# Optimization experiments

Measured on AMD Instinct MI355X. Metric: run time of the kernel, lower is better.

The kernel has to match this reference:

```python
import jax, jax.numpy as jnp
from jax import lax
import numpy as np

DIM = 96
D_STATE = 16
D_CONV = 4
EXPAND = 2
D_INNER = EXPAND * DIM


def _layernorm(x, g, b, eps=1e-5):
    mu = jnp.mean(x, axis=-1, keepdims=True)
    var = jnp.var(x, axis=-1, keepdims=True)
    return (x - mu) * lax.rsqrt(var + eps) * g + b


def _pssm(x, Wp, cw, cb, A, Dp, Wo):
    # x: (B, L, C)
    Bn, L, _ = x.shape
    xp = x @ Wp                                  # (B, L, 3*d_inner)
    x_conv, delta, BC = jnp.split(xp, 3, axis=-1)
    # causal depthwise conv1d (torch pads d_conv-1 both sides then slices [:L] == left pad)
    xc = lax.conv_general_dilated(
        jnp.transpose(x_conv, (0, 2, 1)), cw, (1,), [(D_CONV - 1, 0)],
        dimension_numbers=('NCH', 'OIH', 'NCH'), feature_group_count=D_INNER)
    xc = jnp.transpose(xc, (0, 2, 1)) + cb       # (B, L, d_inner)
    delta = jax.nn.sigmoid(delta)                # (B, L, d_inner)
    Bm = BC[..., :D_STATE]                       # (B, L, N) input gate
    Cm = BC[..., D_STATE:2 * D_STATE]            # (B, L, N) output gate
    # literal einsum 'bnl,ij->bnil' sums A over j -> row-sums vector
    Asum = jnp.sum(A, axis=1)                    # (N,)
    a = jnp.exp(delta[:, :, None, :] * Asum[None, None, :, None])   # (B,L,N,d)
    bu = (delta * xc)[:, :, None, :] * Bm[..., None]                 # (B,L,N,d)

    def scan_dir(a_, b_):
        def step(h, ab):
            at, bt = ab
            h = at * h + bt
            return h, h
        _, hs = lax.scan(step, jnp.zeros_like(a_[:, 0]),
                         (jnp.moveaxis(a_, 1, 0), jnp.moveaxis(b_, 1, 0)))
        return jnp.moveaxis(hs, 0, 1)            # (B, L, N, d)

    h = scan_dir(a, bu) + scan_dir(a[:, ::-1], bu[:, ::-1])[:, ::-1]
    y = jnp.einsum('blnd,bln->bld', h, Cm) + Dp * xc
    return y @ Wo                                # (B, L, C)


def _forward(x, norm_g, norm_b,
             Wp1, cw1, cb1, A1, Dp1, Wo1, lng1, lnb1,
             Wp2, cw2, cb2, A2, Dp2, Wo2, lng2, lnb2,
             Wf, bf, W1, b1, W2, b2):
    Bn, H, W_, C = x.shape
    res = x
    xn = _layernorm(x, norm_g, norm_b)
    xs = xn.reshape(Bn, H * W_, C)
    f1 = _layernorm(_pssm(xs, Wp1, cw1, cb1, A1, Dp1, Wo1), lng1, lnb1).reshape(Bn, H, W_, C)
    f2 = _layernorm(_pssm(xs, Wp2, cw2, cb2, A2, Dp2, Wo2), lng2, lnb2).reshape(Bn, H, W_, C)
    EPS = 1e-12
    n1 = f1 / jnp.maximum(jnp.linalg.norm(f1, axis=-1, keepdims=True), EPS)
    n2 = f2 / jnp.maximum(jnp.linalg.norm(f2, axis=-1, keepdims=True), EPS)
    sim = jnp.sum(n1 * n2, axis=-1, keepdims=True)          # (B,H,W,1)
    fused = sim * f1 + (1.0 - sim) * f2
    cat = jnp.concatenate([f1, fused], axis=-1)             # (B,H,W,2C)
    fc = lax.conv_general_dilated(cat, Wf, (1, 1), 'SAME',
                                  dimension_numbers=('NHWC', 'HWIO', 'NHWC')) + bf
    fc = jax.nn.gelu(fc, approximate=False)
    y = jax.nn.gelu(fc @ W1 + b1, approximate=False) @ W2 + b2
    return y + res


def setup_inputs() -> dict:
    key = jax.random.key(0)
    ks = jax.random.split(key, 32)
    B, H, W, C = 2, 64, 64, DIM

    def n(k, shape, s=1.0):
        return jax.random.normal(k, shape, dtype=jnp.float32) * s

    inp = {}
    inp['x'] = n(ks[0], (B, H, W, C))
    inp['norm_g'] = jnp.ones((C,), jnp.float32)
    inp['norm_b'] = jnp.zeros((C,), jnp.float32)
    for i, off in enumerate([1, 10]):
        p = str(i + 1)
        inp['Wp' + p] = n(ks[off], (C, 3 * D_INNER), 0.02)
        inp['cw' + p] = n(ks[off + 1], (D_INNER, 1, D_CONV), 0.1)
        inp['cb' + p] = jnp.zeros((D_INNER,), jnp.float32)
        # negative A row-sums keep exp(delta*Asum) < 1 -> stable scan over L=4096
        inp['A' + p] = -jnp.abs(n(ks[off + 2], (D_STATE, D_STATE))) * 0.1
        inp['Dp' + p] = n(ks[off + 3], (D_INNER,), 0.1)
        inp['Wo' + p] = n(ks[off + 4], (D_INNER, C), 0.02)
        inp['lng' + p] = jnp.ones((C,), jnp.float32)
        inp['lnb' + p] = jnp.zeros((C,), jnp.float32)
    inp['Wf'] = n(ks[20], (3, 3, 2 * C, C), 0.02)
    inp['bf'] = jnp.zeros((C,), jnp.float32)
    inp['W1'] = n(ks[21], (C, 4 * C), 0.02)
    inp['b1'] = jnp.zeros((4 * C,), jnp.float32)
    inp['W2'] = n(ks[22], (4 * C, C), 0.02)
    inp['b2'] = jnp.zeros((C,), jnp.float32)
    return inp


def reference(x, norm_g, norm_b,
              Wp1, cw1, cb1, A1, Dp1, Wo1, lng1, lnb1,
              Wp2, cw2, cb2, A2, Dp2, Wo2, lng2, lnb2,
              Wf, bf, W1, b1, W2, b2):
    return _forward(x, norm_g, norm_b,
                    Wp1, cw1, cb1, A1, Dp1, Wo1, lng1, lnb1,
                    Wp2, cw2, cb2, A2, Dp2, Wo2, lng2, lnb2,
                    Wf, bf, W1, b1, W2, b2)
```

## Files before the change

kernel.cpp:

```cpp
#include <hip/hip_runtime.h>
#include <hip/hip_bf16.h>
#include <math.h>

#define L_SEQ 4096
#define CDIM 96
#define DIN 192
#define NST 16
#define NCHUNK 64
#define CHLEN 64
#define MROWS 8192
#define XPW2 960
#define SCAN_GRID 3072

typedef __attribute__((ext_vector_type(8))) short bf16x8;
typedef __attribute__((ext_vector_type(4))) float f32x4;
typedef __attribute__((ext_vector_type(4))) short s16x4;
typedef __attribute__((ext_vector_type(4))) unsigned short u16x4;

__device__ __forceinline__ float gelu_exact(float x) {
    return 0.5f * x * (1.0f + erff(x * 0.70710678118654752f));
}

__device__ __forceinline__ float fast_exp2(float x) {
#if __has_builtin(__builtin_amdgcn_exp2f)
    return __builtin_amdgcn_exp2f(x);
#else
    return exp2f(x);
#endif
}

__device__ __forceinline__ float b2f(unsigned short u) {
    return __uint_as_float((unsigned int)u << 16);
}

__device__ __forceinline__ float rowsum16(float s) {
    asm("v_add_f32_dpp %0, %0, %0 row_ror:8 row_mask:0xf bank_mask:0xf" : "+v"(s));
    asm("v_add_f32_dpp %0, %0, %0 row_ror:4 row_mask:0xf bank_mask:0xf" : "+v"(s));
    asm("v_add_f32_dpp %0, %0, %0 row_ror:2 row_mask:0xf bank_mask:0xf" : "+v"(s));
    asm("v_add_f32_dpp %0, %0, %0 row_ror:1 row_mask:0xf bank_mask:0xf" : "+v"(s));
    return s;
}

__device__ __forceinline__ unsigned short f2bf_bits(float f) {
    __hip_bfloat16 h = __float2bfloat16(f);
    return *reinterpret_cast<unsigned short*>(&h);
}

#define CVT_BLOCKS 1440
__global__ __launch_bounds__(256) void prep_kernel(
    const float* __restrict__ Wp0, const float* __restrict__ Wp1,
    const float* __restrict__ Wo0, const float* __restrict__ Wo1,
    const float* __restrict__ Wf, const float* __restrict__ W1, const float* __restrict__ W2,
    __hip_bfloat16* __restrict__ wpT, __hip_bfloat16* __restrict__ wo0T,
    __hip_bfloat16* __restrict__ wo1T, __hip_bfloat16* __restrict__ wfT,
    __hip_bfloat16* __restrict__ w1T, __hip_bfloat16* __restrict__ w2T,
    const float* __restrict__ x, const float* __restrict__ g, const float* __restrict__ b,
    __hip_bfloat16* __restrict__ xn) {
    if (blockIdx.x >= CVT_BLOCKS) {
        int wave = threadIdx.x >> 6;
        int lane = threadIdx.x & 63;
        int row = (blockIdx.x - CVT_BLOCKS) * 4 + wave;
        if (row >= MROWS) return;
        const float* p = x + (size_t)row * CDIM;
        float x0 = p[lane];
        float x1 = (lane < 32) ? p[64 + lane] : 0.f;
        float s = x0 + x1, sq = x0 * x0 + x1 * x1;
#pragma unroll
        for (int o = 32; o >= 1; o >>= 1) { s += __shfl_xor(s, o); sq += __shfl_xor(sq, o); }
        float mean = s * (1.f / 96.f);
        float var = sq * (1.f / 96.f) - mean * mean;
        float w = rsqrtf(var + 1e-5f);
        __hip_bfloat16* q = xn + (size_t)row * CDIM;
        q[lane] = __float2bfloat16((x0 - mean) * w * g[lane] + b[lane]);
        if (lane < 32) q[64 + lane] = __float2bfloat16((x1 - mean) * w * g[64 + lane] + b[64 + lane]);
        return;
    }
    int i = blockIdx.x * 256 + threadIdx.x;
    const int S_WPALL = XPW2 * 96;
    const int S_WO = 96 * 192;
    const int S_WF = 96 * 1728;
    const int S_W1 = 384 * 96;
    const int S_W2 = 96 * 384;
    if (i < S_WPALL) {
        int j = i / 96, r = i % 96;
        int br = j / 480, cc = j % 480;
        const float* W = br ? Wp1 : Wp0;
        wpT[i] = __float2bfloat16(cc < 416 ? W[r * 576 + cc] : 0.f);
        return;
    }
    i -= S_WPALL;
    if (i < S_WO) { int c = i / 192, r = i % 192; wo0T[i] = __float2bfloat16(Wo0[r * 96 + c]); return; }
    i -= S_WO;
    if (i < S_WO) { int c = i / 192, r = i % 192; wo1T[i] = __float2bfloat16(Wo1[r * 96 + c]); return; }
    i -= S_WO;
    if (i < S_WF) { int c = i / 1728, k = i % 1728; wfT[i] = __float2bfloat16(Wf[k * 96 + c]); return; }
    i -= S_WF;
    if (i < S_W1) { int c = i / 96, r = i % 96; w1T[i] = __float2bfloat16(W1[r * 384 + c]); return; }
    i -= S_W1;
    if (i < S_W2) { int c = i / 384, r = i % 384; w2T[i] = __float2bfloat16(W2[r * 96 + c]); return; }
}

template <int MI, int NI, int WR, int WC, int K, int KS, int EPI, typename CT>
__global__ __launch_bounds__(WR * WC * KS * 64) void gemm_direct(
    const __hip_bfloat16* __restrict__ A, int lda,
    const __hip_bfloat16* __restrict__ BT,
    CT* __restrict__ C, int ldc, int N,
    const float* __restrict__ bias, const float* __restrict__ res) {
    __shared__ float part[KS > 1 ? (WR * MI * 16) * (WC * NI * 16) : 1];
    int tid = threadIdx.x;
    int lane = tid & 63, wid = tid >> 6;
    int wk = wid / (WR * WC);
    int wrem = wid % (WR * WC);
    int wm = wrem % WR, wn = wrem / WR;
    int m0 = blockIdx.y * (WR * MI * 16) + wm * MI * 16;
    int n0 = blockIdx.x * (WC * NI * 16) + wn * NI * 16;
    int lr = lane & 15, kh = (lane >> 4) * 8;
    constexpr int KC = K / KS;
    f32x4 acc[MI][NI] = {};
    const __hip_bfloat16* Ap = A + (size_t)(m0 + lr) * lda + kh + wk * KC;
    const __hip_bfloat16* Bp = BT + (size_t)(n0 + lr) * K + kh + wk * KC;
#pragma unroll
    for (int k0 = 0; k0 < KC; k0 += 32) {
        bf16x8 af[MI], bf[NI];
#pragma unroll
        for (int i = 0; i < MI; ++i)
            af[i] = *reinterpret_cast<const bf16x8*>(Ap + (size_t)i * 16 * lda + k0);
#pragma unroll
        for (int j = 0; j < NI; ++j)
            bf[j] = *reinterpret_cast<const bf16x8*>(Bp + (size_t)j * 16 * K + k0);
#pragma unroll
        for (int i = 0; i < MI; ++i)
#pragma unroll
            for (int j = 0; j < NI; ++j)
                acc[i][j] = __builtin_amdgcn_mfma_f32_16x16x32_bf16(af[i], bf[j], acc[i][j], 0, 0, 0);
    }
    int cr = (lane >> 4) << 2;
    if (KS > 1) {
        constexpr int BN = WC * NI * 16;
        if (wk == 1) {
#pragma unroll
            for (int i = 0; i < MI; ++i)
#pragma unroll
                for (int j = 0; j < NI; ++j)
#pragma unroll
                    for (int q = 0; q < 4; ++q)
                        part[(wm * MI * 16 + i * 16 + cr + q) * BN + wn * NI * 16 + j * 16 + lr] =
                            acc[i][j][q];
        }
        __syncthreads();
        if (wk != 0) return;
#pragma unroll
        for (int i = 0; i < MI; ++i)
#pragma unroll
            for (int j = 0; j < NI; ++j)
#pragma unroll
                for (int q = 0; q < 4; ++q)
                    acc[i][j][q] +=
                        part[(wm * MI * 16 + i * 16 + cr + q) * BN + wn * NI * 16 + j * 16 + lr];
    }
#pragma unroll
    for (int i = 0; i < MI; ++i) {
        int row = m0 + i * 16 + cr;
#pragma unroll
        for (int j = 0; j < NI; ++j) {
            int col = n0 + j * 16 + lr;
            if (col < N) {
#pragma unroll
                for (int q = 0; q < 4; ++q) {
                    float v = acc[i][j][q];
                    if (EPI == 1) v = gelu_exact(v + bias[col]);
                    else if (EPI == 2) v = v + bias[col] + res[(size_t)(row + q) * ldc + col];
                    C[(size_t)(row + q) * ldc + col] = (CT)v;
                }
            }
        }
    }
}

__global__ __launch_bounds__(256) void gemm_wo_ln_fuse(
    const __hip_bfloat16* __restrict__ A,
    const __hip_bfloat16* __restrict__ BT0, const __hip_bfloat16* __restrict__ BT1,
    const float* __restrict__ g0, const float* __restrict__ b0,
    const float* __restrict__ g1, const float* __restrict__ b1,
    __hip_bfloat16* __restrict__ cat) {
    int tid = threadIdx.x;
    int lane = tid & 63, wid = tid >> 6;
    int wm = wid & 1, wn = wid >> 1;
    int m0 = blockIdx.x * 32 + wm * 16;
    int n0 = wn * 48;
    int lr = lane & 15, kh = (lane >> 4) * 8;
    f32x4 acc0[3] = {}, acc1[3] = {};
    const __hip_bfloat16* A0 = A + (size_t)(m0 + lr) * 192 + kh;
    const __hip_bfloat16* A1 = A + (size_t)(MROWS + m0 + lr) * 192 + kh;
    const __hip_bfloat16* Bp0 = BT0 + (size_t)(n0 + lr) * 192 + kh;
    const __hip_bfloat16* Bp1 = BT1 + (size_t)(n0 + lr) * 192 + kh;
#pragma unroll
    for (int k0 = 0; k0 < 192; k0 += 32) {
        bf16x8 af0 = *reinterpret_cast<const bf16x8*>(A0 + k0);
        bf16x8 af1 = *reinterpret_cast<const bf16x8*>(A1 + k0);
#pragma unroll
        for (int j = 0; j < 3; ++j) {
            bf16x8 b0v = *reinterpret_cast<const bf16x8*>(Bp0 + (size_t)j * 16 * 192 + k0);
            bf16x8 b1v = *reinterpret_cast<const bf16x8*>(Bp1 + (size_t)j * 16 * 192 + k0);
            acc0[j] = __builtin_amdgcn_mfma_f32_16x16x32_bf16(af0, b0v, acc0[j], 0, 0, 0);
            acc1[j] = __builtin_amdgcn_mfma_f32_16x16x32_bf16(af1, b1v, acc1[j], 0, 0, 0);
        }
    }
    __shared__ float ct0[32][100], ct1[32][100];
    int cr = (lane >> 4) << 2;
#pragma unroll
    for (int j = 0; j < 3; ++j)
#pragma unroll
        for (int q = 0; q < 4; ++q) {
            ct0[wm * 16 + cr + q][n0 + j * 16 + lr] = acc0[j][q];
            ct1[wm * 16 + cr + q][n0 + j * 16 + lr] = acc1[j][q];
        }
    __syncthreads();
#pragma unroll
    for (int rr = 0; rr < 8; ++rr) {
        int row = wid * 8 + rr;
        float a0 = ct0[row][lane];
        float a1 = (lane < 32) ? ct0[row][64 + lane] : 0.f;
        float c0 = ct1[row][lane];
        float c1 = (lane < 32) ? ct1[row][64 + lane] : 0.f;
        float s0 = a0 + a1, q0 = a0 * a0 + a1 * a1;
        float s1 = c0 + c1, q1 = c0 * c0 + c1 * c1;
#pragma unroll
        for (int o = 32; o >= 1; o >>= 1) {
            s0 += __shfl_xor(s0, o); q0 += __shfl_xor(q0, o);
            s1 += __shfl_xor(s1, o); q1 += __shfl_xor(q1, o);
        }
        float mu0 = s0 * (1.f / 96.f), w0 = rsqrtf(q0 * (1.f / 96.f) - mu0 * mu0 + 1e-5f);
        float mu1 = s1 * (1.f / 96.f), w1 = rsqrtf(q1 * (1.f / 96.f) - mu1 * mu1 + 1e-5f);
        float f1a = (a0 - mu0) * w0 * g0[lane] + b0[lane];
        float f2a = (c0 - mu1) * w1 * g1[lane] + b1[lane];
        float f1b = 0.f, f2b = 0.f;
        if (lane < 32) {
            f1b = (a1 - mu0) * w0 * g0[64 + lane] + b0[64 + lane];
            f2b = (c1 - mu1) * w1 * g1[64 + lane] + b1[64 + lane];
        }
        float s11 = f1a * f1a + f1b * f1b;
        float s22 = f2a * f2a + f2b * f2b;
        float s12 = f1a * f2a + f1b * f2b;
#pragma unroll
        for (int o = 32; o >= 1; o >>= 1) {
            s11 += __shfl_xor(s11, o);
            s22 += __shfl_xor(s22, o);
            s12 += __shfl_xor(s12, o);
        }
        float nr1 = fmaxf(sqrtf(s11), 1e-12f);
        float nr2 = fmaxf(sqrtf(s22), 1e-12f);
        float sim = s12 / (nr1 * nr2);
        size_t grow = (size_t)blockIdx.x * 32 + row;
        __hip_bfloat16* q = cat + grow * 192;
        q[lane] = __float2bfloat16(f1a);
        q[96 + lane] = __float2bfloat16(sim * f1a + (1.f - sim) * f2a);
        if (lane < 32) {
            q[64 + lane] = __float2bfloat16(f1b);
            q[96 + 64 + lane] = __float2bfloat16(sim * f1b + (1.f - sim) * f2b);
        }
    }
}

__global__ __launch_bounds__(512) void conv3x3_direct(const __hip_bfloat16* __restrict__ cat,
                                                      const __hip_bfloat16* __restrict__ WfT,
                                                      const float* __restrict__ bfv,
                                                      __hip_bfloat16* __restrict__ out) {
    __shared__ float part[32][96];
    int tid = threadIdx.x;
    int lane = tid & 63, wid = tid >> 6;
    int wm = wid & 1, wn = (wid >> 1) & 1, wk = wid >> 2;
    int m0 = blockIdx.x * 32 + wm * 16;
    int n0 = wn * 48;
    int lr = lane & 15, kh = (lane >> 4) * 8;
    int m = m0 + lr;
    int bb = m >> 12, l = m & 4095, yy = l >> 6, xx = l & 63;
    f32x4 acc[3] = {};
    const __hip_bfloat16* Bp = WfT + (size_t)(n0 + lr) * 1728 + kh;
#pragma unroll
    for (int tap = 0; tap < 9; ++tap) {
        if ((tap & 1) != wk) continue;
        int ky = tap / 3, kx = tap % 3;
        int iy = yy + ky - 1, ix = xx + kx - 1;
        bool ok = ((unsigned)iy < 64u) && ((unsigned)ix < 64u);
        const __hip_bfloat16* Ap = cat + ((size_t)bb * 4096 + (size_t)(iy * 64 + ix)) * 192 + kh;
        int kbase = tap * 192;
#pragma unroll
        for (int kc = 0; kc < 192; kc += 32) {
            bf16x8 af = {};
            if (ok) af = *reinterpret_cast<const bf16x8*>(Ap + kc);
#pragma unroll
            for (int j = 0; j < 3; ++j) {
                bf16x8 bf = *reinterpret_cast<const bf16x8*>(Bp + (size_t)j * 16 * 1728 + kbase + kc);
                acc[j] = __builtin_amdgcn_mfma_f32_16x16x32_bf16(af, bf, acc[j], 0, 0, 0);
            }
        }
    }
    int cr = (lane >> 4) << 2;
    if (wk == 1) {
#pragma unroll
        for (int j = 0; j < 3; ++j)
#pragma unroll
            for (int q = 0; q < 4; ++q)
                part[wm * 16 + cr + q][n0 + j * 16 + lr] = acc[j][q];
    }
    __syncthreads();
    if (wk != 0) return;
    int crow = m0 + cr;
#pragma unroll
    for (int j = 0; j < 3; ++j) {
        int ccol = n0 + j * 16 + lr;
#pragma unroll
        for (int q = 0; q < 4; ++q) {
            float v = acc[j][q] + part[wm * 16 + cr + q][ccol];
            v = gelu_exact(v + bfv[ccol]);
            out[(size_t)(crow + q) * 96 + ccol] = __float2bfloat16(v);
        }
    }
}

__global__ __launch_bounds__(256) void scan_pass1f(
    const __hip_bfloat16* __restrict__ xpw,
    const float* __restrict__ cw0, const float* __restrict__ cw1,
    const float* __restrict__ cb0, const float* __restrict__ cb1,
    const float* __restrict__ A0, const float* __restrict__ A1,
    float* __restrict__ Pc, float* __restrict__ Hf, float* __restrict__ Gb) {
    __shared__ unsigned short rawxu[67][16];
    __shared__ float2 sdx[CHLEN][16];
    __shared__ float sb[CHLEN][16];
    __shared__ float asumv[16];
    int bid = (blockIdx.x & 7) * (SCAN_GRID / 8) + (blockIdx.x >> 3);
    int dg = bid % 12;
    int c = (bid / 12) % NCHUNK;
    int b = (bid / (12 * NCHUNK)) & 1;
    int p = bid / (12 * NCHUNK * 2);
    const float* cw = p ? cw1 : cw0;
    const float* cbp = p ? cb1 : cb0;
    const float* Am = p ? A1 : A0;
    int tid = threadIdx.x;
    if (tid < 16) {
        const float4* Ap4 = (const float4*)(Am + tid * 16);
        float4 a0 = Ap4[0], a1 = Ap4[1], a2 = Ap4[2], a3 = Ap4[3];
        float s = (a0.x + a0.y + a0.z + a0.w) + (a1.x + a1.y + a1.z + a1.w) +
                  (a2.x + a2.y + a2.z + a2.w) + (a3.x + a3.y + a3.z + a3.w);
        asumv[tid] = s * 1.44269504f;
    }
    const unsigned short* xu = (const unsigned short*)xpw;
    int xb = p * 480;
    int t0 = c * CHLEN;
    int r = tid >> 2, q = (tid & 3) * 4;
    size_t grow = (size_t)b * L_SEQ + t0 + r;
    const unsigned short* rowp = xu + grow * XPW2 + xb;
    *(u16x4*)&rawxu[r + 3][q] = *(const u16x4*)(rowp + dg * 16 + q);
    u16x4 dvu = *(const u16x4*)(rowp + 192 + dg * 16 + q);
    u16x4 bvu = *(const u16x4*)(rowp + 384 + q);
    float4 bf4 = {b2f(bvu.x), b2f(bvu.y), b2f(bvu.z), b2f(bvu.w)};
    *(float4*)&sb[r][q] = bf4;
    if (tid < 12) {
        int rr = tid >> 2, qq = (tid & 3) * 4;
        int src = t0 - 3 + rr;
        u16x4 v = {0, 0, 0, 0};
        if (src >= 0)
            v = *(const u16x4*)(xu + ((size_t)b * L_SEQ + src) * XPW2 + xb + dg * 16 + qq);
        *(u16x4*)&rawxu[rr][qq] = v;
    }
    __syncthreads();
    float dd[4] = {b2f(dvu.x), b2f(dvu.y), b2f(dvu.z), b2f(dvu.w)};
#pragma unroll
    for (int i = 0; i < 4; ++i) {
        int d = dg * 16 + q + i;
        float4 w = *(const float4*)(cw + (size_t)d * 4);
        float xc = cbp[d] + w.w * b2f(rawxu[r + 3][q + i]) + w.z * b2f(rawxu[r + 2][q + i]) +
                   w.y * b2f(rawxu[r + 1][q + i]) + w.x * b2f(rawxu[r][q + i]);
        float ds = 1.f / (1.f + __expf(-dd[i]));
        sdx[r][q + i] = make_float2(ds, ds * xc);
    }
    __syncthreads();
    int n = tid & 15, drow = tid >> 4;
    float asum2 = asumv[n];
    float h = 0.f, gb = 0.f, Q = 1.f;
#pragma unroll 4
    for (int t = 0; t < CHLEN; ++t) {
        float2 dx = sdx[t][drow];
        float bm = sb[t][n];
        float a = fast_exp2(dx.x * asum2);
        float bu = dx.y * bm;
        h = a * h + bu;
        gb += Q * bu;
        Q *= a;
    }
    size_t cidx = ((((size_t)p * 2 + b) * NST + n) * DIN + dg * 16 + drow) * NCHUNK + c;
    Pc[cidx] = Q;
    Hf[cidx] = h;
    Gb[cidx] = gb;
}

__global__ __launch_bounds__(256) void scan_pass2(const float* __restrict__ Pc,
                                                  const float* __restrict__ Hf,
                                                  const float* __restrict__ Gb,
                                                  float* __restrict__ Hinf,
                                                  float* __restrict__ Hinb) {
    int t = blockIdx.x * 256 + threadIdx.x;
    if (t >= 2 * 2 * NST * DIN) return;
    size_t base = (size_t)t * NCHUNK;
    {
        float4 P4[16], H4[16];
        const float4* Pp = (const float4*)(Pc + base);
        const float4* Hp = (const float4*)(Hf + base);
#pragma unroll
        for (int i = 0; i < 16; ++i) { P4[i] = Pp[i]; H4[i] = Hp[i]; }
        float hin = 0.f;
        float4* Op = (float4*)(Hinf + base);
#pragma unroll
        for (int i = 0; i < 16; ++i) {
            float4 o;
            o.x = hin; hin = H4[i].x + P4[i].x * hin;
            o.y = hin; hin = H4[i].y + P4[i].y * hin;
            o.z = hin; hin = H4[i].z + P4[i].z * hin;
            o.w = hin; hin = H4[i].w + P4[i].w * hin;
            Op[i] = o;
        }
    }
    {
        float4 P4[16], G4[16];
        const float4* Pp = (const float4*)(Pc + base);
        const float4* Gp = (const float4*)(Gb + base);
#pragma unroll
        for (int i = 0; i < 16; ++i) { P4[i] = Pp[i]; G4[i] = Gp[i]; }
        float gin = 0.f;
        float4* Op = (float4*)(Hinb + base);
#pragma unroll
        for (int i = 15; i >= 0; --i) {
            float4 o;
            o.w = gin; gin = G4[i].w + P4[i].w * gin;
            o.z = gin; gin = G4[i].z + P4[i].z * gin;
            o.y = gin; gin = G4[i].y + P4[i].y * gin;
            o.x = gin; gin = G4[i].x + P4[i].x * gin;
            Op[i] = o;
        }
    }
}

__global__ __launch_bounds__(512) void scan_pass3f(
    const __hip_bfloat16* __restrict__ xpw,
    const float* __restrict__ cw0, const float* __restrict__ cw1,
    const float* __restrict__ cb0, const float* __restrict__ cb1,
    const float* __restrict__ A0, const float* __restrict__ A1,
    const float* __restrict__ Hinf, const float* __restrict__ Hinb,
    const float* __restrict__ Dp0, const float* __restrict__ Dp1,
    __hip_bfloat16* __restrict__ y) {
    __shared__ unsigned short rawxu[67][16];
    __shared__ float2 sdx[CHLEN][16];
    __shared__ float2 sbc[CHLEN][16];
    __shared__ unsigned short sxcu[CHLEN][16];
    __shared__ float ysf[CHLEN][16], ysb[CHLEN][16];
    __shared__ float asumv[16];
    int bid = (blockIdx.x & 7) * (SCAN_GRID / 8) + (blockIdx.x >> 3);
    int dg = bid % 12;
    int c = (bid / 12) % NCHUNK;
    int b = (bid / (12 * NCHUNK)) & 1;
    int p = bid / (12 * NCHUNK * 2);
    const float* cw = p ? cw1 : cw0;
    const float* cbp = p ? cb1 : cb0;
    const float* Am = p ? A1 : A0;
    const float* Dp = p ? Dp1 : Dp0;
    int tid = threadIdx.x;
    if (tid < 16) {
        const float4* Ap4 = (const float4*)(Am + tid * 16);
        float4 a0 = Ap4[0], a1 = Ap4[1], a2 = Ap4[2], a3 = Ap4[3];
        float s = (a0.x + a0.y + a0.z + a0.w) + (a1.x + a1.y + a1.z + a1.w) +
                  (a2.x + a2.y + a2.z + a2.w) + (a3.x + a3.y + a3.z + a3.w);
        asumv[tid] = s * 1.44269504f;
    }
    const unsigned short* xu = (const unsigned short*)xpw;
    int xb = p * 480;
    int t0 = c * CHLEN;
    int r = tid >> 2, q = (tid & 3) * 4;
    u16x4 dvu = {0, 0, 0, 0};
    if (tid < 256) {
        size_t grow = (size_t)b * L_SEQ + t0 + r;
        const unsigned short* rowp = xu + grow * XPW2 + xb;
        *(u16x4*)&rawxu[r + 3][q] = *(const u16x4*)(rowp + dg * 16 + q);
        dvu = *(const u16x4*)(rowp + 192 + dg * 16 + q);
        u16x4 bvu = *(const u16x4*)(rowp + 384 + q);
        u16x4 cvu = *(const u16x4*)(rowp + 400 + q);
        sbc[r][q + 0] = make_float2(b2f(bvu.x), b2f(cvu.x));
        sbc[r][q + 1] = make_float2(b2f(bvu.y), b2f(cvu.y));
        sbc[r][q + 2] = make_float2(b2f(bvu.z), b2f(cvu.z));
        sbc[r][q + 3] = make_float2(b2f(bvu.w), b2f(cvu.w));
        if (tid < 12) {
            int rr = tid >> 2, qq = (tid & 3) * 4;
            int src = t0 - 3 + rr;
            u16x4 v = {0, 0, 0, 0};
            if (src >= 0)
                v = *(const u16x4*)(xu + ((size_t)b * L_SEQ + src) * XPW2 + xb + dg * 16 + qq);
            *(u16x4*)&rawxu[rr][qq] = v;
        }
    }
    __syncthreads();
    if (tid < 256) {
        float dd[4] = {b2f(dvu.x), b2f(dvu.y), b2f(dvu.z), b2f(dvu.w)};
#pragma unroll
        for (int i = 0; i < 4; ++i) {
            int d = dg * 16 + q + i;
            float4 w = *(const float4*)(cw + (size_t)d * 4);
            float xc = cbp[d] + w.w * b2f(rawxu[r + 3][q + i]) + w.z * b2f(rawxu[r + 2][q + i]) +
                       w.y * b2f(rawxu[r + 1][q + i]) + w.x * b2f(rawxu[r][q + i]);
            float ds = 1.f / (1.f + __expf(-dd[i]));
            sdx[r][q + i] = make_float2(ds, ds * xc);
            sxcu[r][q + i] = f2bf_bits(xc);
        }
    }
    __syncthreads();
    int lane = tid & 63, wave = tid >> 6;
    int dir = wave >> 2;
    int wl = wave & 3;
    int n = lane & 15;
    int dloc = wl * 4 + (lane >> 4);
    int d = dg * 16 + dloc;
    float asum2 = asumv[n];
    size_t cidx = ((((size_t)p * 2 + b) * NST + n) * DIN + d) * NCHUNK + c;
    if (dir == 0) {
        float h = Hinf[cidx];
#pragma unroll 4
        for (int t = 0; t < CHLEN; ++t) {
            float2 dx = sdx[t][dloc];
            float2 bc = sbc[t][n];
            float a = fast_exp2(dx.x * asum2);
            h = a * h + dx.y * bc.x;
            float pf = rowsum16(bc.y * h);
            if (n == 0) ysf[t][dloc] = pf;
        }
    } else {
        float gv = Hinb[cidx];
#pragma unroll 4
        for (int t = CHLEN - 1; t >= 0; --t) {
            float2 dx = sdx[t][dloc];
            float2 bc = sbc[t][n];
            float a = fast_exp2(dx.x * asum2);
            gv = a * gv + dx.y * bc.x;
            float pb = rowsum16(bc.y * gv);
            if (n == 0) ysb[t][dloc] = pb;
        }
    }
    __syncthreads();
    if (tid < 256) {
        int tl = tid >> 2, qq = (tid & 3) * 4;
        int d2 = dg * 16 + qq;
        float4 Dv = *(const float4*)(Dp + d2);
        float vs[4];
#pragma unroll
        for (int i = 0; i < 4; ++i)
            vs[i] = ysf[tl][qq + i] + ysb[tl][qq + i] +
                    ((const float*)&Dv)[i] * b2f(sxcu[tl][qq + i]);
        s16x4 pk = {(short)f2bf_bits(vs[0]), (short)f2bf_bits(vs[1]),
                    (short)f2bf_bits(vs[2]), (short)f2bf_bits(vs[3])};
        size_t row = (size_t)b * L_SEQ + t0 + tl;
        *(s16x4*)((unsigned short*)y + ((size_t)p * MROWS + row) * DIN + d2) = pk;
    }
}

extern "C" void kernel_launch(void* const* d_in, const int* in_sizes, int n_in,
                              void* d_out, int out_size, void* d_ws, size_t ws_size,
                              hipStream_t stream) {
    const float* x = (const float*)d_in[0];
    const float* norm_g = (const float*)d_in[1];
    const float* norm_b = (const float*)d_in[2];
    const float* Wp[2] = {(const float*)d_in[3], (const float*)d_in[11]};
    const float* cw[2] = {(const float*)d_in[4], (const float*)d_in[12]};
    const float* cb[2] = {(const float*)d_in[5], (const float*)d_in[13]};
    const float* Ab[2] = {(const float*)d_in[6], (const float*)d_in[14]};
    const float* Dpb[2] = {(const float*)d_in[7], (const float*)d_in[15]};
    const float* Wo[2] = {(const float*)d_in[8], (const float*)d_in[16]};
    const float* lng[2] = {(const float*)d_in[9], (const float*)d_in[17]};
    const float* lnb[2] = {(const float*)d_in[10], (const float*)d_in[18]};
    const float* Wf = (const float*)d_in[19];
    const float* bfv = (const float*)d_in[20];
    const float* W1 = (const float*)d_in[21];
    const float* b1 = (const float*)d_in[22];
    const float* W2 = (const float*)d_in[23];
    const float* b2 = (const float*)d_in[24];
    float* out = (float*)d_out;

    char* base = (char*)d_ws;
    size_t off = 0;
    auto alloc = [&](size_t bytes) { void* p = base + off; off += (bytes + 255) & ~(size_t)255; return p; };
    __hip_bfloat16* xpw = (__hip_bfloat16*)alloc((size_t)MROWS * XPW2 * 2);
    const size_t csz = (size_t)2 * 2 * NST * DIN * NCHUNK;
    float* Pc = (float*)alloc(csz * 4);
    float* Hfc = (float*)alloc(csz * 4);
    float* Gbc = (float*)alloc(csz * 4);
    float* Hinf = (float*)alloc(csz * 4);
    float* Hinb = (float*)alloc(csz * 4);
    __hip_bfloat16* xn_bf = (__hip_bfloat16*)alloc((size_t)MROWS * 96 * 2);
    __hip_bfloat16* yb_bf = (__hip_bfloat16*)alloc((size_t)2 * MROWS * DIN * 2);
    __hip_bfloat16* cat_bf = (__hip_bfloat16*)alloc((size_t)MROWS * DIN * 2);
    __hip_bfloat16* fc_bf = (__hip_bfloat16*)alloc((size_t)MROWS * 96 * 2);
    __hip_bfloat16* h1_bf = (__hip_bfloat16*)alloc((size_t)MROWS * 384 * 2);
    __hip_bfloat16* wpT = (__hip_bfloat16*)alloc((size_t)XPW2 * 96 * 2);
    __hip_bfloat16* woT[2] = {(__hip_bfloat16*)alloc(96 * 192 * 2),
                              (__hip_bfloat16*)alloc(96 * 192 * 2)};
    __hip_bfloat16* wfT = (__hip_bfloat16*)alloc(96 * 1728 * 2);
    __hip_bfloat16* w1T = (__hip_bfloat16*)alloc(384 * 96 * 2);
    __hip_bfloat16* w2T = (__hip_bfloat16*)alloc(96 * 384 * 2);
    (void)ws_size; (void)in_sizes; (void)n_in; (void)out_size;

    prep_kernel<<<dim3(CVT_BLOCKS + 2048), dim3(256), 0, stream>>>(
        Wp[0], Wp[1], Wo[0], Wo[1], Wf, W1, W2,
        wpT, woT[0], woT[1], wfT, w1T, w2T, x, norm_g, norm_b, xn_bf);
    gemm_direct<2, 3, 2, 2, 96, 1, 0, __hip_bfloat16><<<dim3(10, 128), dim3(256), 0, stream>>>(
        xn_bf, 96, wpT, xpw, XPW2, XPW2, nullptr, nullptr);
    scan_pass1f<<<dim3(SCAN_GRID), dim3(256), 0, stream>>>(
        xpw, cw[0], cw[1], cb[0], cb[1], Ab[0], Ab[1], Pc, Hfc, Gbc);
    scan_pass2<<<dim3(48), dim3(256), 0, stream>>>(Pc, Hfc, Gbc, Hinf, Hinb);
    scan_pass3f<<<dim3(SCAN_GRID), dim3(512), 0, stream>>>(
        xpw, cw[0], cw[1], cb[0], cb[1], Ab[0], Ab[1], Hinf, Hinb, Dpb[0], Dpb[1], yb_bf);
    gemm_wo_ln_fuse<<<dim3(256), dim3(256), 0, stream>>>(
        yb_bf, woT[0], woT[1], lng[0], lnb[0], lng[1], lnb[1], cat_bf);
    conv3x3_direct<<<dim3(256), dim3(512), 0, stream>>>(cat_bf, wfT, bfv, fc_bf);
    gemm_direct<2, 3, 2, 2, 96, 1, 1, __hip_bfloat16><<<dim3(4, 128), dim3(256), 0, stream>>>(
        fc_bf, 96, w1T, h1_bf, 384, 384, b1, nullptr);
    gemm_direct<1, 3, 2, 2, 384, 2, 2, float><<<dim3(1, 256), dim3(512), 0, stream>>>(
        h1_bf, 384, w2T, out, 96, 96, b2, x);
}
```

Before: 152.9 us.

## Tile weight transposes via LDS and double grid parallelism for Wo and conv kernels

Weight conversion in prep_kernel now transposes 32x32 tiles through shared memory, so both the global reads and the writes are coalesced instead of strided per element. gemm_wo_ln_fuse is reorganised so each block handles 16 rows, with waves split across the two branches rather than across rows. conv3x3_direct now uses 16-row blocks with a 4-way K split over taps and channel chunks, reduced through shared memory. Both kernels launch twice as many blocks, which gives more parallelism on the 256-CU device, at the cost of re-reading the weights more often per row.

Measured after the change: 149.3 us. -2.4%, faster.

```diff
diff --git a/kernel.cpp b/kernel.cpp
--- a/kernel.cpp
+++ b/kernel.cpp
@@ -46,7 +46,7 @@
     return *reinterpret_cast<unsigned short*>(&h);
 }
 
-#define CVT_BLOCKS 1440
+#define TP_BLOCKS 360
 __global__ __launch_bounds__(256) void prep_kernel(
     const float* __restrict__ Wp0, const float* __restrict__ Wp1,
     const float* __restrict__ Wo0, const float* __restrict__ Wo1,
@@ -56,48 +56,56 @@
     __hip_bfloat16* __restrict__ w1T, __hip_bfloat16* __restrict__ w2T,
     const float* __restrict__ x, const float* __restrict__ g, const float* __restrict__ b,
     __hip_bfloat16* __restrict__ xn) {
-    if (blockIdx.x >= CVT_BLOCKS) {
-        int wave = threadIdx.x >> 6;
-        int lane = threadIdx.x & 63;
-        int row = (blockIdx.x - CVT_BLOCKS) * 4 + wave;
-        if (row >= MROWS) return;
-        const float* p = x + (size_t)row * CDIM;
-        float x0 = p[lane];
-        float x1 = (lane < 32) ? p[64 + lane] : 0.f;
-        float s = x0 + x1, sq = x0 * x0 + x1 * x1;
-#pragma unroll
-        for (int o = 32; o >= 1; o >>= 1) { s += __shfl_xor(s, o); sq += __shfl_xor(sq, o); }
-        float mean = s * (1.f / 96.f);
-        float var = sq * (1.f / 96.f) - mean * mean;
-        float w = rsqrtf(var + 1e-5f);
-        __hip_bfloat16* q = xn + (size_t)row * CDIM;
-        q[lane] = __float2bfloat16((x0 - mean) * w * g[lane] + b[lane]);
-        if (lane < 32) q[64 + lane] = __float2bfloat16((x1 - mean) * w * g[64 + lane] + b[64 + lane]);
+    int tid = threadIdx.x;
+    if (blockIdx.x < TP_BLOCKS) {
+        int t = blockIdx.x;
+        const float* S;
+        __hip_bfloat16* D;
+        int ldS, Cv, Rs;
+        if (t < 45) { S = Wp0; D = wpT; ldS = 576; Cv = 416; Rs = 96; }
+        else if (t < 90) { t -= 45; S = Wp1; D = wpT + 480 * 96; ldS = 576; Cv = 416; Rs = 96; }
+        else if (t < 108) { t -= 90; S = Wo0; D = wo0T; ldS = 96; Cv = 96; Rs = 192; }
+        else if (t < 126) { t -= 108; S = Wo1; D = wo1T; ldS = 96; Cv = 96; Rs = 192; }
+        else if (t < 288) { t -= 126; S = Wf; D = wfT; ldS = 96; Cv = 96; Rs = 1728; }
+        else if (t < 324) { t -= 288; S = W1; D = w1T; ldS = 384; Cv = 384; Rs = 96; }
+        else { t -= 324; S = W2; D = w2T; ldS = 96; Cv = 96; Rs = 384; }
+        int tilesJ = Rs >> 5;
+        int ti = t / tilesJ, tj = t - ti * tilesJ;
+        int c0 = ti * 32, r0 = tj * 32;
+        __shared__ __hip_bfloat16 lt[32][33];
+        int cl = tid & 31, rl = tid >> 5;
+#pragma unroll
+        for (int e = 0; e < 4; ++e) {
+            int row = r0 + rl + e * 8;
+            int col = c0 + cl;
+            float v = (col < Cv) ? S[(size_t)row * ldS + col] : 0.f;
+            lt[cl][rl + e * 8] = __float2bfloat16(v);
+        }
+        __syncthreads();
+#pragma unroll
+        for (int e = 0; e < 4; ++e) {
+            int drow = c0 + rl + e * 8;
+            int dcol = r0 + cl;
+            D[(size_t)drow * Rs + dcol] = lt[rl + e * 8][cl];
+        }
         return;
     }
-    int i = blockIdx.x * 256 + threadIdx.x;
-    const int S_WPALL = XPW2 * 96;
-    const int S_WO = 96 * 192;
-    const int S_WF = 96 * 1728;
-    const int S_W1 = 384 * 96;
-    const int S_W2 = 96 * 384;
-    if (i < S_WPALL) {
-        int j = i / 96, r = i % 96;
-        int br = j / 480, cc = j % 480;
-        const float* W = br ? Wp1 : Wp0;
-        wpT[i] = __float2bfloat16(cc < 416 ? W[r * 576 + cc] : 0.f);
-        return;
-    }
-    i -= S_WPALL;
-    if (i < S_WO) { int c = i / 192, r = i % 192; wo0T[i] = __float2bfloat16(Wo0[r * 96 + c]); return; }
-    i -= S_WO;
-    if (i < S_WO) { int c = i / 192, r = i % 192; wo1T[i] = __float2bfloat16(Wo1[r * 96 + c]); return; }
-    i -= S_WO;
-    if (i < S_WF) { int c = i / 1728, k = i % 1728; wfT[i] = __float2bfloat16(Wf[k * 96 + c]); return; }
-    i -= S_WF;
-    if (i < S_W1) { int c = i / 96, r = i % 96; w1T[i] = __float2bfloat16(W1[r * 384 + c]); return; }
-    i -= S_W1;
-    if (i < S_W2) { int c = i / 384, r = i % 384; w2T[i] = __float2bfloat16(W2[r * 96 + c]); return; }
+    int wave = tid >> 6;
+    int lane = tid & 63;
+    int row = (blockIdx.x - TP_BLOCKS) * 4 + wave;
+    if (row >= MROWS) return;
+    const float* p = x + (size_t)row * CDIM;
+    float x0 = p[lane];
+    float x1 = (lane < 32) ? p[64 + lane] : 0.f;
+    float s = x0 + x1, sq = x0 * x0 + x1 * x1;
+#pragma unroll
+    for (int o = 32; o >= 1; o >>= 1) { s += __shfl_xor(s, o); sq += __shfl_xor(sq, o); }
+    float mean = s * (1.f / 96.f);
+    float var = sq * (1.f / 96.f) - mean * mean;
+    float w = rsqrtf(var + 1e-5f);
+    __hip_bfloat16* q = xn + (size_t)row * CDIM;
+    q[lane] = __float2bfloat16((x0 - mean) * w * g[lane] + b[lane]);
+    if (lane < 32) q[64 + lane] = __float2bfloat16((x1 - mean) * w * g[64 + lane] + b[64 + lane]);
 }
 
 template <int MI, int NI, int WR, int WC, int K, int KS, int EPI, typename CT>
@@ -185,44 +193,38 @@
     __hip_bfloat16* __restrict__ cat) {
     int tid = threadIdx.x;
     int lane = tid & 63, wid = tid >> 6;
-    int wm = wid & 1, wn = wid >> 1;
-    int m0 = blockIdx.x * 32 + wm * 16;
+    int wn = wid & 1, wb = wid >> 1;
+    int m0 = blockIdx.x * 16;
     int n0 = wn * 48;
     int lr = lane & 15, kh = (lane >> 4) * 8;
-    f32x4 acc0[3] = {}, acc1[3] = {};
-    const __hip_bfloat16* A0 = A + (size_t)(m0 + lr) * 192 + kh;
-    const __hip_bfloat16* A1 = A + (size_t)(MROWS + m0 + lr) * 192 + kh;
-    const __hip_bfloat16* Bp0 = BT0 + (size_t)(n0 + lr) * 192 + kh;
-    const __hip_bfloat16* Bp1 = BT1 + (size_t)(n0 + lr) * 192 + kh;
+    f32x4 acc[3] = {};
+    const __hip_bfloat16* Ap = A + (size_t)((wb ? MROWS : 0) + m0 + lr) * 192 + kh;
+    const __hip_bfloat16* BT = wb ? BT1 : BT0;
+    const __hip_bfloat16* Bp = BT + (size_t)(n0 + lr) * 192 + kh;
 #pragma unroll
     for (int k0 = 0; k0 < 192; k0 += 32) {
-        bf16x8 af0 = *reinterpret_cast<const bf16x8*>(A0 + k0);
-        bf16x8 af1 = *reinterpret_cast<const bf16x8*>(A1 + k0);
+        bf16x8 af = *reinterpret_cast<const bf16x8*>(Ap + k0);
 #pragma unroll
         for (int j = 0; j < 3; ++j) {
-            bf16x8 b0v = *reinterpret_cast<const bf16x8*>(Bp0 + (size_t)j * 16 * 192 + k0);
-            bf16x8 b1v = *reinterpret_cast<const bf16x8*>(Bp1 + (size_t)j * 16 * 192 + k0);
-            acc0[j] = __builtin_amdgcn_mfma_f32_16x16x32_bf16(af0, b0v, acc0[j], 0, 0, 0);
-            acc1[j] = __builtin_amdgcn_mfma_f32_16x16x32_bf16(af1, b1v, acc1[j], 0, 0, 0);
-        }
-    }
-    __shared__ float ct0[32][100], ct1[32][100];
+            bf16x8 bv = *reinterpret_cast<const bf16x8*>(Bp + (size_t)j * 16 * 192 + k0);
+            acc[j] = __builtin_amdgcn_mfma_f32_16x16x32_bf16(af, bv, acc[j], 0, 0, 0);
+        }
+    }
+    __shared__ float ct[2][16][100];
     int cr = (lane >> 4) << 2;
 #pragma unroll
     for (int j = 0; j < 3; ++j)
 #pragma unroll
-        for (int q = 0; q < 4; ++q) {
-            ct0[wm * 16 + cr + q][n0 + j * 16 + lr] = acc0[j][q];
-            ct1[wm * 16 + cr + q][n0 + j * 16 + lr] = acc1[j][q];
-        }
+        for (int q = 0; q < 4; ++q)
+            ct[wb][cr + q][n0 + j * 16 + lr] = acc[j][q];
     __syncthreads();
 #pragma unroll
-    for (int rr = 0; rr < 8; ++rr) {
-        int row = wid * 8 + rr;
-        float a0 = ct0[row][lane];
-        float a1 = (lane < 32) ? ct0[row][64 + lane] : 0.f;
-        float c0 = ct1[row][lane];
-        float c1 = (lane < 32) ? ct1[row][64 + lane] : 0.f;
+    for (int rr = 0; rr < 4; ++rr) {
+        int row = wid * 4 + rr;
+        float a0 = ct[0][row][lane];
+        float a1 = (lane < 32) ? ct[0][row][64 + lane] : 0.f;
+        float c0 = ct[1][row][lane];
+        float c1 = (lane < 32) ? ct[1][row][64 + lane] : 0.f;
         float s0 = a0 + a1, q0 = a0 * a0 + a1 * a1;
         float s1 = c0 + c1, q1 = c0 * c0 + c1 * c1;
 #pragma unroll
@@ -251,7 +253,7 @@
         float nr1 = fmaxf(sqrtf(s11), 1e-12f);
         float nr2 = fmaxf(sqrtf(s22), 1e-12f);
         float sim = s12 / (nr1 * nr2);
-        size_t grow = (size_t)blockIdx.x * 32 + row;
+        size_t grow = (size_t)blockIdx.x * 16 + row;
         __hip_bfloat16* q = cat + grow * 192;
         q[lane] = __float2bfloat16(f1a);
         q[96 + lane] = __float2bfloat16(sim * f1a + (1.f - sim) * f2a);
@@ -266,55 +268,53 @@
                                                       const __hip_bfloat16* __restrict__ WfT,
                                                       const float* __restrict__ bfv,
                                                       __hip_bfloat16* __restrict__ out) {
-    __shared__ float part[32][96];
+    __shared__ float part[3][16][100];
     int tid = threadIdx.x;
     int lane = tid & 63, wid = tid >> 6;
-    int wm = wid & 1, wn = (wid >> 1) & 1, wk = wid >> 2;
-    int m0 = blockIdx.x * 32 + wm * 16;
+    int wn = wid & 1, wk = wid >> 1;
+    int m0 = blockIdx.x * 16;
     int n0 = wn * 48;
     int lr = lane & 15, kh = (lane >> 4) * 8;
     int m = m0 + lr;
     int bb = m >> 12, l = m & 4095, yy = l >> 6, xx = l & 63;
     f32x4 acc[3] = {};
     const __hip_bfloat16* Bp = WfT + (size_t)(n0 + lr) * 1728 + kh;
-#pragma unroll
-    for (int tap = 0; tap < 9; ++tap) {
-        if ((tap & 1) != wk) continue;
-        int ky = tap / 3, kx = tap % 3;
+    for (int u = wk; u < 54; u += 4) {
+        int tap = u / 6;
+        int kc = (u - tap * 6) * 32;
+        int ky = tap / 3, kx = tap - ky * 3;
         int iy = yy + ky - 1, ix = xx + kx - 1;
         bool ok = ((unsigned)iy < 64u) && ((unsigned)ix < 64u);
-        const __hip_bfloat16* Ap = cat + ((size_t)bb * 4096 + (size_t)(iy * 64 + ix)) * 192 + kh;
-        int kbase = tap * 192;
-#pragma unroll
-        for (int kc = 0; kc < 192; kc += 32) {
-            bf16x8 af = {};
-            if (ok) af = *reinterpret_cast<const bf16x8*>(Ap + kc);
-#pragma unroll
-            for (int j = 0; j < 3; ++j) {
-                bf16x8 bf = *reinterpret_cast<const bf16x8*>(Bp + (size_t)j * 16 * 1728 + kbase + kc);
-                acc[j] = __builtin_amdgcn_mfma_f32_16x16x32_bf16(af, bf, acc[j], 0, 0, 0);
-            }
+        bf16x8 af = {};
+        if (ok)
+            af = *reinterpret_cast<const bf16x8*>(
+                cat + ((size_t)bb * 4096 + (size_t)(iy * 64 + ix)) * 192 + kh + kc);
+        int kbase = tap * 192 + kc;
+#pragma unroll
+        for (int j = 0; j < 3; ++j) {
+            bf16x8 bfr = *reinterpret_cast<const bf16x8*>(Bp + (size_t)j * 16 * 1728 + kbase);
+            acc[j] = __builtin_amdgcn_mfma_f32_16x16x32_bf16(af, bfr, acc[j], 0, 0, 0);
         }
     }
     int cr = (lane >> 4) << 2;
-    if (wk == 1) {
+    if (wk != 0) {
 #pragma unroll
         for (int j = 0; j < 3; ++j)
 #pragma unroll
             for (int q = 0; q < 4; ++q)
-                part[wm * 16 + cr + q][n0 + j * 16 + lr] = acc[j][q];
+                part[wk - 1][cr + q][n0 + j * 16 + lr] = acc[j][q];
     }
     __syncthreads();
     if (wk != 0) return;
-    int crow = m0 + cr;
 #pragma unroll
     for (int j = 0; j < 3; ++j) {
         int ccol = n0 + j * 16 + lr;
 #pragma unroll
         for (int q = 0; q < 4; ++q) {
-            float v = acc[j][q] + part[wm * 16 + cr + q][ccol];
+            float v = acc[j][q] + part[0][cr + q][ccol] + part[1][cr + q][ccol] +
+                      part[2][cr + q][ccol];
             v = gelu_exact(v + bfv[ccol]);
-            out[(size_t)(crow + q) * 96 + ccol] = __float2bfloat16(v);
+            out[(size_t)(m0 + cr + q) * 96 + ccol] = __float2bfloat16(v);
         }
     }
 }
@@ -605,7 +605,7 @@
     __hip_bfloat16* w2T = (__hip_bfloat16*)alloc(96 * 384 * 2);
     (void)ws_size; (void)in_sizes; (void)n_in; (void)out_size;
 
-    prep_kernel<<<dim3(CVT_BLOCKS + 2048), dim3(256), 0, stream>>>(
+    prep_kernel<<<dim3(TP_BLOCKS + 2048), dim3(256), 0, stream>>>(
         Wp[0], Wp[1], Wo[0], Wo[1], Wf, W1, W2,
         wpT, woT[0], woT[1], wfT, w1T, w2T, x, norm_g, norm_b, xn_bf);
     gemm_direct<2, 3, 2, 2, 96, 1, 0, __hip_bfloat16><<<dim3(10, 128), dim3(256), 0, stream>>>(
@@ -615,9 +615,9 @@
     scan_pass2<<<dim3(48), dim3(256), 0, stream>>>(Pc, Hfc, Gbc, Hinf, Hinb);
     scan_pass3f<<<dim3(SCAN_GRID), dim3(512), 0, stream>>>(
         xpw, cw[0], cw[1], cb[0], cb[1], Ab[0], Ab[1], Hinf, Hinb, Dpb[0], Dpb[1], yb_bf);
-    gemm_wo_ln_fuse<<<dim3(256), dim3(256), 0, stream>>>(
+    gemm_wo_ln_fuse<<<dim3(512), dim3(256), 0, stream>>>(
         yb_bf, woT[0], woT[1], lng[0], lnb[0], lng[1], lnb[1], cat_bf);
-    conv3x3_direct<<<dim3(256), dim3(512), 0, stream>>>(cat_bf, wfT, bfv, fc_bf);
+    conv3x3_direct<<<dim3(512), dim3(512), 0, stream>>>(cat_bf, wfT, bfv, fc_bf);
     gemm_direct<2, 3, 2, 2, 96, 1, 1, __hip_bfloat16><<<dim3(4, 128), dim3(256), 0, stream>>>(
         fc_bf, 96, w1T, h1_bf, 384, 384, b1, nullptr);
     gemm_direct<1, 3, 2, 2, 384, 2, 2, float><<<dim3(1, 256), dim3(512), 0, stream>>>(
```
